# Kernel optimization log

Hardware: AMD Instinct MI355X
Metric: run time of the kernel (lower is better)

## Reference

```python
import jax, jax.numpy as jnp
import numpy as np

NUM_CLASSES = 1000
TEMPERATURE = 0.1
B, B_OOD, D = 4096, 4096, 512


def _l2norm(x):
    return x / jnp.linalg.norm(x, axis=-1, keepdims=True)


def setup_inputs() -> dict:
    key = jax.random.key(0)
    k1, k2, k3, k4, k5 = jax.random.split(key, 5)
    return {
        "centers1": _l2norm(jax.random.normal(k1, (NUM_CLASSES, D), dtype=jnp.float32)),
        "features": _l2norm(jax.random.normal(k2, (B, D), dtype=jnp.float32)),
        "targets": jax.random.randint(k3, (B,), 0, NUM_CLASSES, dtype=jnp.int64 if jax.config.jax_enable_x64 else jnp.int32),
        "features_ood": _l2norm(jax.random.normal(k4, (B_OOD, D), dtype=jnp.float32)),
        "pseudo_target_ood": jax.random.randint(k5, (B_OOD,), 0, NUM_CLASSES, dtype=jnp.int64 if jax.config.jax_enable_x64 else jnp.int32),
    }


def reference(centers1, features, targets, features_ood, pseudo_target_ood):
    C = centers1.shape[0]
    b = features.shape[0]
    bo = features_ood.shape[0]
    n = b + C + bo  # total anchors: batch + class centers + ood

    centers_lbl = jnp.arange(C, dtype=targets.dtype)
    ood_lbl = jnp.full((bo,), C, dtype=targets.dtype)  # ood gets label == num_classes
    targets_all = jnp.concatenate([targets, centers_lbl, ood_lbl])              # [N]
    targets_all_class = jnp.concatenate([targets, centers_lbl, pseudo_target_ood])  # [N]

    # per-class count over all N labels (pseudo labels for ood)
    batch_cls_count = jnp.zeros((C,), dtype=jnp.float32).at[targets_all_class].add(1.0)

    # positive mask: same label as anchor, excluding self (diagonal for j < B)
    mask = (targets_all[:b, None] == targets_all[None, :]).astype(jnp.float32)  # [B,N]
    logits_mask = 1.0 - (jnp.arange(n)[None, :] == jnp.arange(b)[:, None]).astype(jnp.float32)
    mask = mask * logits_mask

    features_all = jnp.concatenate([features, centers1, features_ood], axis=0)  # [N,D]
    logits = jnp.matmul(features, features_all.T) / TEMPERATURE                 # [B,N]
    logits = logits - jax.lax.stop_gradient(jnp.max(logits, axis=1, keepdims=True))

    exp_logits = jnp.exp(logits) * logits_mask
    # class-balanced per-instance weight (count of the column's class, minus positive mask)
    per_ins_weight = batch_cls_count[targets_all_class][None, :] - mask         # [B,N]
    exp_logits_sum = jnp.sum(exp_logits / per_ins_weight, axis=1, keepdims=True)
    log_prob = logits - jnp.log(exp_logits_sum)

    mean_log_prob_pos = jnp.sum(mask * log_prob, axis=1) / jnp.sum(mask, axis=1)
    loss = -jnp.mean(mean_log_prob_pos)
    return loss
```

## Files before the change

### kernel.cpp

```cpp
#include <hip/hip_runtime.h>
#include <stdint.h>

#define NUM_C 1000
#define NB    4096
#define NCOL  9192
#define NPAD  9216
#define DK    512
#define BM    128
#define BN    256
#define INV_T 10.0f

typedef __attribute__((ext_vector_type(4))) float f32x4;

#define OFF_FALL  0u
#define OFF_CNT   4718592u
#define OFF_CNTT  4722688u
#define OFF_S     4726784u
#define OFF_P     4743168u

__device__ __forceinline__ void async16(const void* g, void* l) {
  __builtin_amdgcn_global_load_lds((const __attribute__((address_space(1))) void*)g,
                                   (__attribute__((address_space(3))) void*)l,
                                   16, 0, 0);
}

__device__ __forceinline__ unsigned sw_e4m3(float x) {
  float ax = fabsf(x);
  unsigned s = (__float_as_uint(x) >> 24) & 0x80u;
  if (ax < 0.015625f) {
    int n = (int)rintf(ax * 512.0f);
    if (n >= 8) return s | 0x08u;
    return s | (unsigned)n;
  }
  if (ax >= 448.0f) return s | 0x7Eu;
  unsigned u = __float_as_uint(ax);
  int ee = (int)(u >> 23) - 127;
  float scale = __uint_as_float((unsigned)(3 - ee + 127) << 23);
  int qv = (int)rintf(ax * scale);
  if (qv == 16) { ee++; qv = 8; }
  return s | (unsigned)(((ee + 7) << 3) | (qv - 8));
}

template <bool HI>
__device__ __forceinline__ int cvt2(float a, float b, int old) {
#if __has_builtin(__builtin_amdgcn_cvt_pk_fp8_f32)
  return __builtin_amdgcn_cvt_pk_fp8_f32(a, b, old, HI);
#else
  unsigned pk = sw_e4m3(a) | (sw_e4m3(b) << 8);
  return HI ? (int)(((unsigned)old & 0x0000FFFFu) | (pk << 16))
            : (int)(((unsigned)old & 0xFFFF0000u) | pk);
#endif
}

__device__ __forceinline__ long long mk_ll(unsigned lo, unsigned hi) {
  return (long long)(((unsigned long long)hi << 32) | lo);
}

__global__ __launch_bounds__(256) void prep_k(const float* __restrict__ centers,
                                              const float* __restrict__ feats,
                                              const float* __restrict__ ood,
                                              const int* __restrict__ targets,
                                              const int* __restrict__ pseudo,
                                              uint4* __restrict__ fall,
                                              unsigned* __restrict__ cnt,
                                              unsigned* __restrict__ cntT,
                                              float* __restrict__ SP) {
  __shared__ unsigned hc[1024];
  __shared__ unsigned hct[1024];
  const int tid = threadIdx.x;

  int idx  = blockIdx.x * 256 + tid;
  int lane = idx & 63;
  int kp   = (idx >> 6) & 7;
  int t    = idx >> 9;
  int row  = t * 16 + (lane & 15);
  int k0   = kp * 64 + (lane >> 4) * 8;

  const float* src = nullptr;
  if (row < NB)              src = feats   + (size_t)row * DK;
  else if (row < NB + NUM_C) src = centers + (size_t)(row - NB) * DK;
  else if (row < NCOL)       src = ood     + (size_t)(row - NB - NUM_C) * DK;
  uint4 out = make_uint4(0u, 0u, 0u, 0u);
  if (src) {
    float4 v0 = *(const float4*)(src + k0);
    float4 v1 = *(const float4*)(src + k0 + 4);
    float4 v2 = *(const float4*)(src + k0 + 32);
    float4 v3 = *(const float4*)(src + k0 + 36);
    int p;
    p = 0; p = cvt2<false>(v0.x, v0.y, p); p = cvt2<true>(v0.z, v0.w, p); out.x = (unsigned)p;
    p = 0; p = cvt2<false>(v1.x, v1.y, p); p = cvt2<true>(v1.z, v1.w, p); out.y = (unsigned)p;
    p = 0; p = cvt2<false>(v2.x, v2.y, p); p = cvt2<true>(v2.z, v2.w, p); out.z = (unsigned)p;
    p = 0; p = cvt2<false>(v3.x, v3.y, p); p = cvt2<true>(v3.z, v3.w, p); out.w = (unsigned)p;
  }
  fall[idx] = out;

  if (blockIdx.x < 16) {
    for (int kk = tid; kk < 1024; kk += 256) { hc[kk] = 0u; hct[kk] = 0u; }
    __syncthreads();
    int i = blockIdx.x * 256 + tid;
    int tt = targets[i];
    atomicAdd(&hc[tt], 1u);
    atomicAdd(&hct[tt], 1u);
    atomicAdd(&hc[pseudo[i]], 1u);
    __syncthreads();
    for (int kk = tid; kk < 1024; kk += 256) {
      unsigned c = hc[kk], ct = hct[kk];
      if (c)  atomicAdd(&cnt[kk], c);
      if (ct) atomicAdd(&cntT[kk], ct);
    }
  } else if (blockIdx.x < 48) {
    SP[(blockIdx.x - 16) * 256 + tid] = 0.0f;
  }
}

__global__ __launch_bounds__(256, 2) void gemm_fused(const unsigned char* __restrict__ fall,
                                                     const int* __restrict__ targets,
                                                     const int* __restrict__ pseudo,
                                                     const unsigned* __restrict__ cnt,
                                                     float* __restrict__ Sacc,
                                                     float* __restrict__ Pacc) {
  __shared__ unsigned char Alds[65536];
  __shared__ int    sLbl[BN];
  __shared__ float  sRw0[BN];
  __shared__ float  sRw1[BN];
  __shared__ int    sTgt[BM];

  const int tid   = threadIdx.x;
  const int nTile = blockIdx.x;
  const int mTile = blockIdx.y;
  const int lane  = tid & 63;
  const int wv    = tid >> 6;
  const int wm    = wv >> 1;
  const int wn    = wv & 1;
  const int q     = lane >> 4;
  const int cIdx  = lane & 15;

  {
    const unsigned char* aSrc = fall + (size_t)(mTile * 8) * 8192;
#pragma unroll
    for (int i = 0; i < 16; i++)
      async16(aSrc + (i * 256 + tid) * 16, &Alds[(i * 256 + tid) * 16]);
  }

  {
    int j = nTile * BN + tid;
    int lbl, tac;
    if (j >= NCOL)         { lbl = -1; tac = -1; }
    else if (j < NB)       { tac = targets[j]; lbl = tac; }
    else if (j < NB+NUM_C) { tac = j - NB;     lbl = tac; }
    else                   { tac = pseudo[j - NB - NUM_C]; lbl = NUM_C; }
    sLbl[tid] = lbl;
    if (tac >= 0) {
      float w = (float)(1u + cnt[tac]);
      sRw0[tid] = 1.0f / w;
      sRw1[tid] = 1.0f / (w - 1.0f);
    } else {
      sRw0[tid] = 0.f;
      sRw1[tid] = 0.f;
    }
    if (tid < BM) sTgt[tid] = targets[mTile * BM + tid];
  }

  f32x4 acc[4][8];
#pragma unroll
  for (int mi = 0; mi < 4; mi++)
#pragma unroll
    for (int ni = 0; ni < 8; ni++)
      acc[mi][ni] = (f32x4){0.f, 0.f, 0.f, 0.f};

  const unsigned char* bBase = fall + (size_t)(nTile * 16 + wn * 8) * 8192 + lane * 16;
  const unsigned aBase = (unsigned)(wm * 4) * 8192u + (unsigned)lane * 16u;

  uint4 bCur[8], bNxt[8];
#pragma unroll
  for (int ni = 0; ni < 8; ni++)
    bCur[ni] = *(const uint4*)(bBase + ni * 8192);

  __syncthreads();

#pragma unroll
  for (int kp = 0; kp < 8; kp++) {
    if (kp < 7) {
#pragma unroll
      for (int ni = 0; ni < 8; ni++)
        bNxt[ni] = *(const uint4*)(bBase + ni * 8192 + (kp + 1) * 1024);
    }
    long long af0[4], af1[4];
#pragma unroll
    for (int mi = 0; mi < 4; mi++) {
      af0[mi] = *(const long long*)&Alds[aBase + mi * 8192 + kp * 1024];
      af1[mi] = *(const long long*)&Alds[aBase + mi * 8192 + kp * 1024 + 8];
    }
#pragma unroll
    for (int mi = 0; mi < 4; mi++)
#pragma unroll
      for (int ni = 0; ni < 8; ni++)
        acc[mi][ni] = __builtin_amdgcn_mfma_f32_16x16x32_fp8_fp8(af0[mi], mk_ll(bCur[ni].x, bCur[ni].y), acc[mi][ni], 0, 0, 0);
#pragma unroll
    for (int mi = 0; mi < 4; mi++)
#pragma unroll
      for (int ni = 0; ni < 8; ni++)
        acc[mi][ni] = __builtin_amdgcn_mfma_f32_16x16x32_fp8_fp8(af1[mi], mk_ll(bCur[ni].z, bCur[ni].w), acc[mi][ni], 0, 0, 0);
    if (kp < 7) {
#pragma unroll
      for (int ni = 0; ni < 8; ni++) bCur[ni] = bNxt[ni];
    }
  }

  float vS[16], vP[16];
#pragma unroll
  for (int s = 0; s < 16; s++) { vS[s] = 0.f; vP[s] = 0.f; }

#pragma unroll
  for (int ni = 0; ni < 8; ni++) {
    int jloc = wn * 128 + ni * 16 + cIdx;
    int j    = nTile * BN + jloc;
    int lblj = sLbl[jloc];
    float rw0 = sRw0[jloc], rw1 = sRw1[jloc];
#pragma unroll
    for (int mi = 0; mi < 4; mi++) {
      f32x4 a = acc[mi][ni];
#pragma unroll
      for (int r = 0; r < 4; r++) {
        int iloc = wm * 64 + mi * 16 + q * 4 + r;
        int i    = mTile * BM + iloc;
        int ti   = sTgt[iloc];
        float l  = a[r] * INV_T;
        bool diag = (j == i);
        bool pos  = (lblj == ti) && !diag;
        float rw  = diag ? 0.0f : (pos ? rw1 : rw0);
        float e   = __expf(l - 10.0f) * rw;
        vS[mi * 4 + r] += e;
        vP[mi * 4 + r] += pos ? l : 0.0f;
      }
    }
  }

#define RED_STEP(m, s, h)                                        \
  {                                                              \
    float sendS = (cIdx & (m)) ? vS[(s)] : vS[(s) + (h)];        \
    float sendP = (cIdx & (m)) ? vP[(s)] : vP[(s) + (h)];        \
    float rS = __shfl_xor(sendS, (m), 64);                       \
    float rP = __shfl_xor(sendP, (m), 64);                       \
    vS[(s)] = ((cIdx & (m)) ? vS[(s) + (h)] : vS[(s)]) + rS;     \
    vP[(s)] = ((cIdx & (m)) ? vP[(s) + (h)] : vP[(s)]) + rP;     \
  }
  RED_STEP(8, 0, 8) RED_STEP(8, 1, 8) RED_STEP(8, 2, 8) RED_STEP(8, 3, 8)
  RED_STEP(8, 4, 8) RED_STEP(8, 5, 8) RED_STEP(8, 6, 8) RED_STEP(8, 7, 8)
  RED_STEP(4, 0, 4) RED_STEP(4, 1, 4) RED_STEP(4, 2, 4) RED_STEP(4, 3, 4)
  RED_STEP(2, 0, 2) RED_STEP(2, 1, 2)
  RED_STEP(1, 0, 1)
#undef RED_STEP

  {
    int rowLoc = wm * 64 + (cIdx >> 2) * 16 + q * 4 + (cIdx & 3);
    int i = mTile * BM + rowLoc;
    atomicAdd(&Sacc[i], vS[0]);
    atomicAdd(&Pacc[i], vP[0]);
  }
}

__global__ __launch_bounds__(256) void finalize_k(const float* __restrict__ S,
                                                  const float* __restrict__ P,
                                                  const int* __restrict__ targets,
                                                  const unsigned* __restrict__ cntT,
                                                  float* __restrict__ out) {
  __shared__ unsigned ct[1024];
  __shared__ float red[4];
  int tid = threadIdx.x;
  for (int k = tid; k < 1024; k += 256) ct[k] = cntT[k];
  __syncthreads();
  float local = 0.f;
  for (int i = tid; i < NB; i += 256) {
    float npos = (float)ct[targets[i]];
    local += P[i] / npos - INV_T - __logf(S[i]);
  }
  for (int m = 1; m < 64; m <<= 1) local += __shfl_xor(local, m, 64);
  if ((tid & 63) == 0) red[tid >> 6] = local;
  __syncthreads();
  if (tid == 0) {
    float t = red[0] + red[1] + red[2] + red[3];
    out[0] = -t / (float)NB;
  }
}

extern "C" void kernel_launch(void* const* d_in, const int* in_sizes, int n_in,
                              void* d_out, int out_size, void* d_ws, size_t ws_size,
                              hipStream_t stream) {
  const float* centers = (const float*)d_in[0];
  const float* feats   = (const float*)d_in[1];
  const int*   targets = (const int*)d_in[2];
  const float* ood     = (const float*)d_in[3];
  const int*   pseudo  = (const int*)d_in[4];

  char* ws = (char*)d_ws;
  uint4*    fall  = (uint4*)(ws + OFF_FALL);
  unsigned* cnt   = (unsigned*)(ws + OFF_CNT);
  unsigned* cntT  = (unsigned*)(ws + OFF_CNTT);
  float*    Sacc  = (float*)(ws + OFF_S);
  float*    Pacc  = (float*)(ws + OFF_P);

  hipMemsetAsync(ws + OFF_CNT, 0, 8192, stream);
  prep_k<<<dim3((NPAD * 32) / 256), 256, 0, stream>>>(centers, feats, ood, targets, pseudo,
                                                      fall, cnt, cntT, Sacc);
  gemm_fused<<<dim3(NPAD / BN, NB / BM), 256, 0, stream>>>((const unsigned char*)fall, targets,
                                                           pseudo, cnt, Sacc, Pacc);
  finalize_k<<<1, 256, 0, stream>>>(Sacc, Pacc, targets, cntT, (float*)d_out);
}
```

Baseline: 119.9 us.

## Use scaled 16x16x128 f8f6f4 MFMA with a 32-byte-per-lane fp8 layout

Replaces the 16x16x32 fp8 MFMA inner loop with the gfx950 scaled 16x16x128 f8f6f4 MFMA, using unit E8M0 scales. The prep kernel is changed to match: each thread now writes 32 contiguous fp8 bytes per lane, so the K slices fit the new operand layout, and the prep grid is halved. This cuts the MFMA instruction count and register shuffling per K step, and makes wider A and B loads. The cost is a changed B prefetch pattern and a dependence on the exact operand layout of the new instruction.

```diff
diff --git a/kernel.cpp b/kernel.cpp
--- a/kernel.cpp
+++ b/kernel.cpp
@@ -11,12 +11,15 @@
 #define INV_T 10.0f
 
 typedef __attribute__((ext_vector_type(4))) float f32x4;
+typedef __attribute__((ext_vector_type(8))) int  v8i;
 
 #define OFF_FALL  0u
 #define OFF_CNT   4718592u
 #define OFF_CNTT  4722688u
 #define OFF_S     4726784u
 #define OFF_P     4743168u
+
+#define SCL 0x7F7F7F7Fu
 
 __device__ __forceinline__ void async16(const void* g, void* l) {
   __builtin_amdgcn_global_load_lds((const __attribute__((address_space(1))) void*)g,
@@ -52,16 +55,12 @@
 #endif
 }
 
-__device__ __forceinline__ long long mk_ll(unsigned lo, unsigned hi) {
-  return (long long)(((unsigned long long)hi << 32) | lo);
-}
-
 __global__ __launch_bounds__(256) void prep_k(const float* __restrict__ centers,
                                               const float* __restrict__ feats,
                                               const float* __restrict__ ood,
                                               const int* __restrict__ targets,
                                               const int* __restrict__ pseudo,
-                                              uint4* __restrict__ fall,
+                                              unsigned char* __restrict__ fall,
                                               unsigned* __restrict__ cnt,
                                               unsigned* __restrict__ cntT,
                                               float* __restrict__ SP) {
@@ -71,28 +70,33 @@
 
   int idx  = blockIdx.x * 256 + tid;
   int lane = idx & 63;
-  int kp   = (idx >> 6) & 7;
-  int t    = idx >> 9;
+  int kb   = (idx >> 6) & 3;
+  int t    = idx >> 8;
   int row  = t * 16 + (lane & 15);
-  int k0   = kp * 64 + (lane >> 4) * 8;
+  int k0   = kb * 128 + (lane >> 4) * 32;
 
   const float* src = nullptr;
   if (row < NB)              src = feats   + (size_t)row * DK;
   else if (row < NB + NUM_C) src = centers + (size_t)(row - NB) * DK;
   else if (row < NCOL)       src = ood     + (size_t)(row - NB - NUM_C) * DK;
-  uint4 out = make_uint4(0u, 0u, 0u, 0u);
+  uint4 o0 = make_uint4(0u, 0u, 0u, 0u), o1 = o0;
   if (src) {
-    float4 v0 = *(const float4*)(src + k0);
-    float4 v1 = *(const float4*)(src + k0 + 4);
-    float4 v2 = *(const float4*)(src + k0 + 32);
-    float4 v3 = *(const float4*)(src + k0 + 36);
-    int p;
-    p = 0; p = cvt2<false>(v0.x, v0.y, p); p = cvt2<true>(v0.z, v0.w, p); out.x = (unsigned)p;
-    p = 0; p = cvt2<false>(v1.x, v1.y, p); p = cvt2<true>(v1.z, v1.w, p); out.y = (unsigned)p;
-    p = 0; p = cvt2<false>(v2.x, v2.y, p); p = cvt2<true>(v2.z, v2.w, p); out.z = (unsigned)p;
-    p = 0; p = cvt2<false>(v3.x, v3.y, p); p = cvt2<true>(v3.z, v3.w, p); out.w = (unsigned)p;
-  }
-  fall[idx] = out;
+    const float4* s4 = (const float4*)(src + k0);
+    unsigned w[8];
+#pragma unroll
+    for (int g = 0; g < 8; g += 2) {
+      float4 va = s4[g], vb = s4[g + 1];
+      int p = 0;
+      p = cvt2<false>(va.x, va.y, p); p = cvt2<true>(va.z, va.w, p); w[g] = (unsigned)p;
+      p = 0;
+      p = cvt2<false>(vb.x, vb.y, p); p = cvt2<true>(vb.z, vb.w, p); w[g + 1] = (unsigned)p;
+    }
+    o0 = make_uint4(w[0], w[1], w[2], w[3]);
+    o1 = make_uint4(w[4], w[5], w[6], w[7]);
+  }
+  uint4* dst = (uint4*)(fall + (size_t)idx * 32);
+  dst[0] = o0;
+  dst[1] = o1;
 
   if (blockIdx.x < 16) {
     for (int kk = tid; kk < 1024; kk += 256) { hc[kk] = 0u; hct[kk] = 0u; }
@@ -168,42 +172,45 @@
     for (int ni = 0; ni < 8; ni++)
       acc[mi][ni] = (f32x4){0.f, 0.f, 0.f, 0.f};
 
-  const unsigned char* bBase = fall + (size_t)(nTile * 16 + wn * 8) * 8192 + lane * 16;
-  const unsigned aBase = (unsigned)(wm * 4) * 8192u + (unsigned)lane * 16u;
-
-  uint4 bCur[8], bNxt[8];
-#pragma unroll
-  for (int ni = 0; ni < 8; ni++)
-    bCur[ni] = *(const uint4*)(bBase + ni * 8192);
+  const unsigned char* bBase = fall + (size_t)(nTile * 16 + wn * 8) * 8192 + lane * 32;
+  const unsigned aOff = (unsigned)(wm * 4) * 8192u + (unsigned)lane * 32u;
+
+  v8i bk0[4], bk1[4];
+#pragma unroll
+  for (int tt = 0; tt < 4; tt++) bk0[tt] = *(const v8i*)(bBase + (size_t)tt * 8192);
+#pragma unroll
+  for (int tt = 0; tt < 4; tt++) bk1[tt] = *(const v8i*)(bBase + (size_t)(4 + tt) * 8192);
 
   __syncthreads();
 
-#pragma unroll
-  for (int kp = 0; kp < 8; kp++) {
-    if (kp < 7) {
-#pragma unroll
-      for (int ni = 0; ni < 8; ni++)
-        bNxt[ni] = *(const uint4*)(bBase + ni * 8192 + (kp + 1) * 1024);
-    }
-    long long af0[4], af1[4];
-#pragma unroll
-    for (int mi = 0; mi < 4; mi++) {
-      af0[mi] = *(const long long*)&Alds[aBase + mi * 8192 + kp * 1024];
-      af1[mi] = *(const long long*)&Alds[aBase + mi * 8192 + kp * 1024 + 8];
+  v8i af[4];
+#pragma unroll
+  for (int h = 0; h < 8; h++) {
+    const int kb = h >> 1;
+    const int g  = h & 1;
+    if (g == 0) {
+#pragma unroll
+      for (int mi = 0; mi < 4; mi++)
+        af[mi] = *(const v8i*)&Alds[aOff + mi * 8192 + kb * 2048];
     }
 #pragma unroll
     for (int mi = 0; mi < 4; mi++)
 #pragma unroll
-      for (int ni = 0; ni < 8; ni++)
-        acc[mi][ni] = __builtin_amdgcn_mfma_f32_16x16x32_fp8_fp8(af0[mi], mk_ll(bCur[ni].x, bCur[ni].y), acc[mi][ni], 0, 0, 0);
-#pragma unroll
-    for (int mi = 0; mi < 4; mi++)
-#pragma unroll
-      for (int ni = 0; ni < 8; ni++)
-        acc[mi][ni] = __builtin_amdgcn_mfma_f32_16x16x32_fp8_fp8(af1[mi], mk_ll(bCur[ni].z, bCur[ni].w), acc[mi][ni], 0, 0, 0);
-    if (kp < 7) {
-#pragma unroll
-      for (int ni = 0; ni < 8; ni++) bCur[ni] = bNxt[ni];
+      for (int tt = 0; tt < 4; tt++) {
+        if (g == 0)
+          acc[mi][tt] = __builtin_amdgcn_mfma_scale_f32_16x16x128_f8f6f4(
+              af[mi], bk0[tt], acc[mi][tt], 0, 0, 0, (int)SCL, 0, (int)SCL);
+        else
+          acc[mi][4 + tt] = __builtin_amdgcn_mfma_scale_f32_16x16x128_f8f6f4(
+              af[mi], bk1[tt], acc[mi][4 + tt], 0, 0, 0, (int)SCL, 0, (int)SCL);
+      }
+    if (h + 2 < 8) {
+      const int nkb = (h + 2) >> 1;
+#pragma unroll
+      for (int tt = 0; tt < 4; tt++) {
+        if (g == 0) bk0[tt] = *(const v8i*)(bBase + (size_t)tt * 8192 + nkb * 2048);
+        else        bk1[tt] = *(const v8i*)(bBase + (size_t)(4 + tt) * 8192 + nkb * 2048);
+      }
     }
   }
 
@@ -294,16 +301,15 @@
   const int*   pseudo  = (const int*)d_in[4];
 
   char* ws = (char*)d_ws;
-  uint4*    fall  = (uint4*)(ws + OFF_FALL);
+  unsigned char* fall = (unsigned char*)(ws + OFF_FALL);
   unsigned* cnt   = (unsigned*)(ws + OFF_CNT);
   unsigned* cntT  = (unsigned*)(ws + OFF_CNTT);
   float*    Sacc  = (float*)(ws + OFF_S);
   float*    Pacc  = (float*)(ws + OFF_P);
 
   hipMemsetAsync(ws + OFF_CNT, 0, 8192, stream);
-  prep_k<<<dim3((NPAD * 32) / 256), 256, 0, stream>>>(centers, feats, ood, targets, pseudo,
-                                                      fall, cnt, cntT, Sacc);
-  gemm_fused<<<dim3(NPAD / BN, NB / BM), 256, 0, stream>>>((const unsigned char*)fall, targets,
-                                                           pseudo, cnt, Sacc, Pacc);
+  prep_k<<<dim3(576), 256, 0, stream>>>(centers, feats, ood, targets, pseudo,
+                                        fall, cnt, cntT, Sacc);
+  gemm_fused<<<dim3(NPAD / BN, NB / BM), 256, 0, stream>>>(fall, targets, pseudo, cnt, Sacc, Pacc);
   finalize_k<<<1, 256, 0, stream>>>(Sacc, Pacc, targets, cntT, (float*)d_out);
 }
```

New measurement: 143.2 us. +19.4%, slower.
